# Kernel tuning notes

Measured on AMD Instinct MI355X. Metric: run time of the kernel, lower is better.

The kernel has to match this reference:

```python
import jax, jax.numpy as jnp
import numpy as np

B, S, H, V, T = 512, 128, 1024, 4096, 32  # batch, enc len, hidden, output_size, max_length


def setup_inputs() -> dict:
    key = jax.random.key(0)
    ks = jax.random.split(key, 9)
    sc = 1.0 / np.sqrt(H).astype(np.float32)
    return {
        "encoder_outputs": jax.random.normal(ks[0], (B, S, H), jnp.float32),
        "sem_embs": jax.random.normal(ks[1], (B, S, H), jnp.float32),
        "embedding": jax.random.normal(ks[2], (V + 3, H), jnp.float32) * sc,
        "W_ih": jax.random.normal(ks[3], (3 * H, H), jnp.float32) * sc,
        "W_hh": jax.random.normal(ks[4], (3 * H, H), jnp.float32) * sc,
        "b_ih": jax.random.normal(ks[5], (3 * H,), jnp.float32) * sc,
        "b_hh": jax.random.normal(ks[6], (3 * H,), jnp.float32) * sc,
        "W_out": jax.random.normal(ks[7], (V, H), jnp.float32) * sc,
        "b_out": jax.random.normal(ks[8], (V,), jnp.float32) * sc,
    }


def gru_cell(x, h, W_ih, W_hh, b_ih, b_hh):
    # PyTorch GRU cell math: r,z,n gate order
    gi = x @ W_ih.T + b_ih
    gh = h @ W_hh.T + b_hh
    i_r, i_z, i_n = jnp.split(gi, 3, axis=-1)
    h_r, h_z, h_n = jnp.split(gh, 3, axis=-1)
    r = jax.nn.sigmoid(i_r + h_r)
    z = jax.nn.sigmoid(i_z + h_z)
    n = jnp.tanh(i_n + r * h_n)
    return (1.0 - z) * n + z * h


def reference(encoder_outputs, sem_embs, embedding, W_ih, W_hh, b_ih, b_hh, W_out, b_out):
    bs, _, hid = encoder_outputs.shape
    # init_batch: append fake EOS key/value embeddings (length mask is all-False -> no-op)
    fake_eos = jnp.broadcast_to(embedding[V][None, None, :], (bs, 1, hid))
    fake_eos_sem = jnp.broadcast_to(embedding[V + 1][None, None, :], (bs, 1, hid))
    keys = jnp.concatenate([encoder_outputs, fake_eos], axis=1)      # [B, S+1, H]
    values = jnp.concatenate([sem_embs, fake_eos_sem], axis=1)       # [B, S+1, H]
    scale = 1.0 / jnp.sqrt(jnp.asarray(hid, jnp.float32))

    def step(carry, _):
        tok, h = carry
        emb = embedding[tok]                                         # [B, H]
        h = gru_cell(emb, h, W_ih, W_hh, b_ih, b_hh)                 # [B, H]
        w = jax.nn.softmax(jnp.einsum('bh,bkh->bk', h, keys) * scale, axis=-1)  # [B, S+1]
        r = jnp.einsum('bk,bkh->bh', w, values)                      # [B, H]
        logits = (r + h) @ W_out.T + b_out                           # [B, V]
        logp = jax.nn.log_softmax(logits, axis=-1)
        x = jnp.argmax(logits, axis=-1)                              # eval-mode greedy decode
        lp = jnp.take_along_axis(logp, x[:, None], axis=-1)[:, 0]
        ent = -jnp.sum(jnp.exp(logp) * logp, axis=-1)
        return (x, h), (x, lp, ent, w)

    tok0 = jnp.full((bs,), V + 2, dtype=jnp.int32)  # SOS token = output_size + 2
    h0 = jnp.zeros((bs, hid), jnp.float32)
    _, (seq, lps, ents, ws) = jax.lax.scan(step, (tok0, h0), None, length=T)
    seq = jnp.moveaxis(seq, 0, 1)    # [B, T]
    lps = jnp.moveaxis(lps, 0, 1)
    ents = jnp.moveaxis(ents, 0, 1)
    ws = jnp.moveaxis(ws, 0, 1)      # [B, T, S+1]
    zf = jnp.zeros((bs, 1), jnp.float32)
    sequence = jnp.concatenate([seq, jnp.zeros((bs, 1), seq.dtype)], axis=-1)
    per_step_logits = jnp.concatenate([lps, zf], axis=-1)
    entropy = jnp.concatenate([ents, zf], axis=-1)
    return sequence, per_step_logits, entropy, ws
```

## Files before the change

### kernel.cpp

```cpp
#include <hip/hip_runtime.h>
#include <stdint.h>

#define HDIM 1024
#define NB   512
#define SEQ  128
#define VOUT 4096
#define TSTEPS 32
#define EROWS 4160

#define SEQ_OFF 0
#define LP_OFF  16896
#define ENT_OFF 33792
#define WS_OFF  50688

__global__ void init_kernel(float* __restrict__ h, int* __restrict__ tok,
                            float* __restrict__ out) {
  int idx = blockIdx.x * blockDim.x + threadIdx.x;
  h[idx] = 0.f;
  if (idx < NB) {
    tok[idx] = VOUT + 2;
    out[SEQ_OFF + idx * 33 + 32] = 0.f;
    out[LP_OFF  + idx * 33 + 32] = 0.f;
    out[ENT_OFF + idx * 33 + 32] = 0.f;
  }
}

__global__ __launch_bounds__(256) void gemm64_kernel(
    const float* __restrict__ A, const float* __restrict__ W,
    const float* __restrict__ bias, float* __restrict__ C,
    int N, int Mlim, int KLEN, int zstride) {
  __shared__ __align__(16) float Als[32][68];
  __shared__ __align__(16) float Bls[32][68];
  const int tid = threadIdx.x;
  const int tx = tid & 15, ty = tid >> 4;
  const int m0 = blockIdx.y * 64, n0 = blockIdx.x * 64;
  const int z = blockIdx.z;
  const int kbeg = z * KLEN;
  const int sr = tid >> 3;
  const int scol = (tid & 7) << 2;

  const int ca0 = sr ^ scol;
  const int ca1 = (sr + 32) ^ scol;

  const int ra = min(m0 + sr, Mlim - 1);
  const int rb = min(m0 + sr + 32, Mlim - 1);
  const float* a0 = A + (size_t)ra * HDIM + kbeg + scol;
  const float* a1 = A + (size_t)rb * HDIM + kbeg + scol;
  const float* w0 = W + (size_t)(n0 + sr) * HDIM + kbeg + scol;
  const float* w1 = W + (size_t)(n0 + sr + 32) * HDIM + kbeg + scol;

  float accT[4][4];
#pragma unroll
  for (int i = 0; i < 4; ++i)
#pragma unroll
    for (int j = 0; j < 4; ++j) accT[i][j] = 0.f;

  float4 av0 = *(const float4*)(a0);
  float4 av1 = *(const float4*)(a1);
  float4 wv0 = *(const float4*)(w0);
  float4 wv1 = *(const float4*)(w1);

  for (int k0 = 0; k0 < KLEN; k0 += 32) {
    __syncthreads();
    Als[scol + 0][ca0] = av0.x; Als[scol + 1][ca0] = av0.y;
    Als[scol + 2][ca0] = av0.z; Als[scol + 3][ca0] = av0.w;
    Als[scol + 0][ca1] = av1.x; Als[scol + 1][ca1] = av1.y;
    Als[scol + 2][ca1] = av1.z; Als[scol + 3][ca1] = av1.w;
    Bls[scol + 0][ca0] = wv0.x; Bls[scol + 1][ca0] = wv0.y;
    Bls[scol + 2][ca0] = wv0.z; Bls[scol + 3][ca0] = wv0.w;
    Bls[scol + 0][ca1] = wv1.x; Bls[scol + 1][ca1] = wv1.y;
    Bls[scol + 2][ca1] = wv1.z; Bls[scol + 3][ca1] = wv1.w;
    __syncthreads();

    {
      const int kn = min(k0 + 32, KLEN - 32);
      av0 = *(const float4*)(a0 + kn);
      av1 = *(const float4*)(a1 + kn);
      wv0 = *(const float4*)(w0 + kn);
      wv1 = *(const float4*)(w1 + kn);
    }

    float ac[4][4];
#pragma unroll
    for (int i = 0; i < 4; ++i)
#pragma unroll
      for (int j = 0; j < 4; ++j) ac[i][j] = 0.f;

#pragma unroll
    for (int kk = 0; kk < 32; ++kk) {
      const int sz = kk & 28;
      float4 a4 = *(const float4*)&Als[kk][(ty * 4) ^ sz];
      float4 b4 = *(const float4*)&Bls[kk][(tx * 4) ^ sz];
      float a_[4] = {a4.x, a4.y, a4.z, a4.w};
      float b_[4] = {b4.x, b4.y, b4.z, b4.w};
#pragma unroll
      for (int i = 0; i < 4; ++i)
#pragma unroll
        for (int j = 0; j < 4; ++j) ac[i][j] = fmaf(a_[i], b_[j], ac[i][j]);
    }
#pragma unroll
    for (int i = 0; i < 4; ++i)
#pragma unroll
      for (int j = 0; j < 4; ++j) accT[i][j] += ac[i][j];
  }

  float* Cz = C + (size_t)z * zstride;
  float b0 = 0.f, b1 = 0.f, b2 = 0.f, b3 = 0.f;
  if (z == 0) {
    b0 = bias[n0 + tx * 4 + 0];
    b1 = bias[n0 + tx * 4 + 1];
    b2 = bias[n0 + tx * 4 + 2];
    b3 = bias[n0 + tx * 4 + 3];
  }
#pragma unroll
  for (int i = 0; i < 4; ++i) {
    int m = m0 + ty * 4 + i;
    float4 o;
    o.x = accT[i][0] + b0;
    o.y = accT[i][1] + b1;
    o.z = accT[i][2] + b2;
    o.w = accT[i][3] + b3;
    *(float4*)&Cz[(size_t)m * N + n0 + tx * 4] = o;
  }
}

__global__ __launch_bounds__(256) void gate_kernel(
    const float* __restrict__ E2, const float* __restrict__ gh,
    const int* __restrict__ tok, float* __restrict__ h) {
  int idx = blockIdx.x * blockDim.x + threadIdx.x;
  int b = idx >> 8;
  int c = (idx & 255) << 2;
  const float* e = E2 + (size_t)tok[b] * (3 * HDIM) + c;
  const float* g0 = gh + (size_t)b * (3 * HDIM) + c;
  const float* g1 = g0 + (size_t)NB * 3 * HDIM;
  float4 ir = *(const float4*)(e);
  float4 iz = *(const float4*)(e + HDIM);
  float4 in_ = *(const float4*)(e + 2 * HDIM);
  float4 hra = *(const float4*)(g0);
  float4 hza = *(const float4*)(g0 + HDIM);
  float4 hna = *(const float4*)(g0 + 2 * HDIM);
  float4 hrb = *(const float4*)(g1);
  float4 hzb = *(const float4*)(g1 + HDIM);
  float4 hnb = *(const float4*)(g1 + 2 * HDIM);
  float4 hv = *(const float4*)&h[(size_t)b * HDIM + c];
  float4 o;
  {
    float r = 1.f / (1.f + expf(-(ir.x + hra.x + hrb.x)));
    float z = 1.f / (1.f + expf(-(iz.x + hza.x + hzb.x)));
    float n = tanhf(in_.x + r * (hna.x + hnb.x));
    o.x = (1.f - z) * n + z * hv.x;
  }
  {
    float r = 1.f / (1.f + expf(-(ir.y + hra.y + hrb.y)));
    float z = 1.f / (1.f + expf(-(iz.y + hza.y + hzb.y)));
    float n = tanhf(in_.y + r * (hna.y + hnb.y));
    o.y = (1.f - z) * n + z * hv.y;
  }
  {
    float r = 1.f / (1.f + expf(-(ir.z + hra.z + hrb.z)));
    float z = 1.f / (1.f + expf(-(iz.z + hza.z + hzb.z)));
    float n = tanhf(in_.z + r * (hna.z + hnb.z));
    o.z = (1.f - z) * n + z * hv.z;
  }
  {
    float r = 1.f / (1.f + expf(-(ir.w + hra.w + hrb.w)));
    float z = 1.f / (1.f + expf(-(iz.w + hza.w + hzb.w)));
    float n = tanhf(in_.w + r * (hna.w + hnb.w));
    o.w = (1.f - z) * n + z * hv.w;
  }
  *(float4*)&h[(size_t)b * HDIM + c] = o;
}

#define SMEM_BYTES 37440
__global__ __launch_bounds__(512) void attn_gh_kernel(
    const float* __restrict__ h, const float* __restrict__ enc,
    const float* __restrict__ sem, const float* __restrict__ emb,
    float* __restrict__ x, float* __restrict__ out, int t,
    const float* __restrict__ W_hh, const float* __restrict__ b_hh,
    float* __restrict__ gh, int nattn) {
  __shared__ __align__(16) char smem[SMEM_BYTES];
  const int tid = threadIdx.x;
  if ((int)blockIdx.x < nattn) {
    float* hs = reinterpret_cast<float*>(smem);
    float (*accb)[HDIM] = reinterpret_cast<float (*)[HDIM]>(smem + 4096);
    float* uls = reinterpret_cast<float*>(smem + 36864);
    float* usums = reinterpret_cast<float*>(smem + 37392);
    const int b = blockIdx.x;
    const int lane = tid & 63, wv = tid >> 6;

    *(float2*)&hs[tid * 2] = *(const float2*)&h[(size_t)b * HDIM + tid * 2];
    __syncthreads();

    const int l4 = lane * 4;
    float4 hv0 = *(const float4*)&hs[l4];
    float4 hv1 = *(const float4*)&hs[l4 + 256];
    float4 hv2 = *(const float4*)&hs[l4 + 512];
    float4 hv3 = *(const float4*)&hs[l4 + 768];

    float4 acc0 = {0, 0, 0, 0}, acc1 = {0, 0, 0, 0};
    float4 acc2 = {0, 0, 0, 0}, acc3 = {0, 0, 0, 0};
    float usum = 0.f;

    for (int k = wv; k < SEQ + 1; k += 8) {
      const float* kr;
      const float* vr;
      if (k < SEQ) {
        kr = enc + ((size_t)b * SEQ + k) * HDIM;
        vr = sem + ((size_t)b * SEQ + k) * HDIM;
      } else {
        kr = emb + (size_t)VOUT * HDIM;
        vr = emb + (size_t)(VOUT + 1) * HDIM;
      }
      float4 e0 = *(const float4*)(kr + l4);
      float4 e1 = *(const float4*)(kr + l4 + 256);
      float4 e2 = *(const float4*)(kr + l4 + 512);
      float4 e3 = *(const float4*)(kr + l4 + 768);
      float4 v0 = *(const float4*)(vr + l4);
      float4 v1 = *(const float4*)(vr + l4 + 256);
      float4 v2 = *(const float4*)(vr + l4 + 512);
      float4 v3 = *(const float4*)(vr + l4 + 768);

      float p = 0.f;
      p = fmaf(e0.x, hv0.x, p); p = fmaf(e0.y, hv0.y, p);
      p = fmaf(e0.z, hv0.z, p); p = fmaf(e0.w, hv0.w, p);
      p = fmaf(e1.x, hv1.x, p); p = fmaf(e1.y, hv1.y, p);
      p = fmaf(e1.z, hv1.z, p); p = fmaf(e1.w, hv1.w, p);
      p = fmaf(e2.x, hv2.x, p); p = fmaf(e2.y, hv2.y, p);
      p = fmaf(e2.z, hv2.z, p); p = fmaf(e2.w, hv2.w, p);
      p = fmaf(e3.x, hv3.x, p); p = fmaf(e3.y, hv3.y, p);
      p = fmaf(e3.z, hv3.z, p); p = fmaf(e3.w, hv3.w, p);
#pragma unroll
      for (int off = 32; off; off >>= 1) p += __shfl_xor(p, off);

      float u = expf(p * 0.03125f);
      usum += u;
      if (lane == 0) uls[k] = u;

      acc0.x = fmaf(u, v0.x, acc0.x); acc0.y = fmaf(u, v0.y, acc0.y);
      acc0.z = fmaf(u, v0.z, acc0.z); acc0.w = fmaf(u, v0.w, acc0.w);
      acc1.x = fmaf(u, v1.x, acc1.x); acc1.y = fmaf(u, v1.y, acc1.y);
      acc1.z = fmaf(u, v1.z, acc1.z); acc1.w = fmaf(u, v1.w, acc1.w);
      acc2.x = fmaf(u, v2.x, acc2.x); acc2.y = fmaf(u, v2.y, acc2.y);
      acc2.z = fmaf(u, v2.z, acc2.z); acc2.w = fmaf(u, v2.w, acc2.w);
      acc3.x = fmaf(u, v3.x, acc3.x); acc3.y = fmaf(u, v3.y, acc3.y);
      acc3.z = fmaf(u, v3.z, acc3.z); acc3.w = fmaf(u, v3.w, acc3.w);
    }

    if (lane == 0) usums[wv] = usum;
    *(float4*)&accb[wv][l4] = acc0;
    *(float4*)&accb[wv][l4 + 256] = acc1;
    *(float4*)&accb[wv][l4 + 512] = acc2;
    *(float4*)&accb[wv][l4 + 768] = acc3;
    __syncthreads();

    float U = 0.f;
#pragma unroll
    for (int w = 0; w < 8; ++w) U += usums[w];
    float rinv = 1.f / U;

#pragma unroll
    for (int dd = 0; dd < 2; ++dd) {
      int d = tid + dd * 512;
      float sum = 0.f;
#pragma unroll
      for (int w = 0; w < 8; ++w) sum += accb[w][d];
      x[(size_t)b * HDIM + d] = sum * rinv + hs[d];
    }

    if (tid < SEQ + 1)
      out[WS_OFF + ((size_t)b * TSTEPS + t) * (SEQ + 1) + tid] = uls[tid] * rinv;
  } else {
    float (*Als)[132] = reinterpret_cast<float (*)[132]>(smem);
    float (*Bls)[68] = reinterpret_cast<float (*)[68]>(smem + 16896);
    int gb = blockIdx.x - nattn;
    const int z = gb / 192; gb -= z * 192;
    const int by = gb / 48, bx = gb - by * 48;
    const int m0 = by * 128, n0 = bx * 64;
    const int kbeg = z * 512;
    const int tx = tid & 15, ty = tid >> 4;
    const int sr = tid >> 3;
    const int scol = (tid & 7) << 2;
    const int ca = sr ^ scol;

    const float* a0 = h + (size_t)(m0 + sr) * HDIM + kbeg + scol;
    const float* a1 = h + (size_t)(m0 + sr + 64) * HDIM + kbeg + scol;
    const float* w0 = W_hh + (size_t)(n0 + sr) * HDIM + kbeg + scol;

    float accT[4][4];
#pragma unroll
    for (int i = 0; i < 4; ++i)
#pragma unroll
      for (int j = 0; j < 4; ++j) accT[i][j] = 0.f;

    float4 av0 = *(const float4*)(a0);
    float4 av1 = *(const float4*)(a1);
    float4 wv0 = *(const float4*)(w0);

    for (int k0 = 0; k0 < 512; k0 += 32) {
      __syncthreads();
      Als[scol + 0][ca] = av0.x; Als[scol + 1][ca] = av0.y;
      Als[scol + 2][ca] = av0.z; Als[scol + 3][ca] = av0.w;
      Als[scol + 0][ca + 64] = av1.x; Als[scol + 1][ca + 64] = av1.y;
      Als[scol + 2][ca + 64] = av1.z; Als[scol + 3][ca + 64] = av1.w;
      Bls[scol + 0][ca] = wv0.x; Bls[scol + 1][ca] = wv0.y;
      Bls[scol + 2][ca] = wv0.z; Bls[scol + 3][ca] = wv0.w;
      __syncthreads();

      {
        const int kn = min(k0 + 32, 512 - 32);
        av0 = *(const float4*)(a0 + kn);
        av1 = *(const float4*)(a1 + kn);
        wv0 = *(const float4*)(w0 + kn);
      }

      float ac[4][4];
#pragma unroll
      for (int i = 0; i < 4; ++i)
#pragma unroll
        for (int j = 0; j < 4; ++j) ac[i][j] = 0.f;

#pragma unroll
      for (int kk = 0; kk < 32; ++kk) {
        const int sz = kk & 28;
        float4 a4 = *(const float4*)&Als[kk][(ty * 4) ^ sz];
        float4 b4 = *(const float4*)&Bls[kk][(tx * 4) ^ sz];
        float a_[4] = {a4.x, a4.y, a4.z, a4.w};
        float b_[4] = {b4.x, b4.y, b4.z, b4.w};
#pragma unroll
        for (int i = 0; i < 4; ++i)
#pragma unroll
          for (int j = 0; j < 4; ++j) ac[i][j] = fmaf(a_[i], b_[j], ac[i][j]);
      }
#pragma unroll
      for (int i = 0; i < 4; ++i)
#pragma unroll
        for (int j = 0; j < 4; ++j) accT[i][j] += ac[i][j];
    }

    float* Cz = gh + (size_t)z * (NB * 3 * HDIM);
    float b0 = 0.f, b1 = 0.f, b2 = 0.f, b3 = 0.f;
    if (z == 0) {
      b0 = b_hh[n0 + tx * 4 + 0];
      b1 = b_hh[n0 + tx * 4 + 1];
      b2 = b_hh[n0 + tx * 4 + 2];
      b3 = b_hh[n0 + tx * 4 + 3];
    }
#pragma unroll
    for (int i = 0; i < 4; ++i) {
      int m = m0 + ty * 4 + i;
      float4 o;
      o.x = accT[i][0] + b0;
      o.y = accT[i][1] + b1;
      o.z = accT[i][2] + b2;
      o.w = accT[i][3] + b3;
      *(float4*)&Cz[(size_t)m * (3 * HDIM) + n0 + tx * 4] = o;
    }
  }
}

__global__ __launch_bounds__(256) void finalgate_kernel(
    const float* __restrict__ logits, float* __restrict__ out, int t,
    const float* __restrict__ E2, const float* __restrict__ gh,
    float* __restrict__ h) {
  const int b = blockIdx.x, tid = threadIdx.x;
  const int lane = tid & 63, wv = tid >> 6;
  const float* lrow = logits + (size_t)b * VOUT;
  float m = -3.4e38f; int mi = 0;
  float s = 0.f, ts = 0.f;
#pragma unroll
  for (int it = 0; it < 4; ++it) {
    int j = (tid << 2) + (it << 10);
    float4 v = *(const float4*)&lrow[j];
    float e;
    e = expf(v.x); s += e; ts = fmaf(e, v.x, ts); if (v.x > m) { m = v.x; mi = j; }
    e = expf(v.y); s += e; ts = fmaf(e, v.y, ts); if (v.y > m) { m = v.y; mi = j + 1; }
    e = expf(v.z); s += e; ts = fmaf(e, v.z, ts); if (v.z > m) { m = v.z; mi = j + 2; }
    e = expf(v.w); s += e; ts = fmaf(e, v.w, ts); if (v.w > m) { m = v.w; mi = j + 3; }
  }
#pragma unroll
  for (int off = 32; off; off >>= 1) {
    float om = __shfl_xor(m, off);
    int oi = __shfl_xor(mi, off);
    s += __shfl_xor(s, off);
    ts += __shfl_xor(ts, off);
    if (om > m || (om == m && oi < mi)) { m = om; mi = oi; }
  }
  __shared__ float smx[4], ssm[4], sts[4];
  __shared__ int smi[4];
  __shared__ int mib;
  if (lane == 0) { smx[wv] = m; smi[wv] = mi; ssm[wv] = s; sts[wv] = ts; }
  __syncthreads();
  if (tid == 0) {
#pragma unroll
    for (int w = 1; w < 4; ++w) {
      s += ssm[w]; ts += sts[w];
      if (smx[w] > m || (smx[w] == m && smi[w] < mi)) { m = smx[w]; mi = smi[w]; }
    }
    float lse = logf(s);
    float lp = m - lse;
    float ent = lse - ts / s;
    out[SEQ_OFF + (size_t)b * 33 + t] = (float)mi;
    out[LP_OFF  + (size_t)b * 33 + t] = lp;
    out[ENT_OFF + (size_t)b * 33 + t] = ent;
    mib = mi;
  }
  __syncthreads();

  const int c = tid << 2;
  const float* e = E2 + (size_t)mib * (3 * HDIM) + c;
  const float* g0 = gh + (size_t)b * (3 * HDIM) + c;
  const float* g1 = g0 + (size_t)NB * 3 * HDIM;
  float4 ir = *(const float4*)(e);
  float4 iz = *(const float4*)(e + HDIM);
  float4 in_ = *(const float4*)(e + 2 * HDIM);
  float4 hra = *(const float4*)(g0);
  float4 hza = *(const float4*)(g0 + HDIM);
  float4 hna = *(const float4*)(g0 + 2 * HDIM);
  float4 hrb = *(const float4*)(g1);
  float4 hzb = *(const float4*)(g1 + HDIM);
  float4 hnb = *(const float4*)(g1 + 2 * HDIM);
  float4 hv = *(const float4*)&h[(size_t)b * HDIM + c];
  float4 o;
  {
    float r = 1.f / (1.f + expf(-(ir.x + hra.x + hrb.x)));
    float z = 1.f / (1.f + expf(-(iz.x + hza.x + hzb.x)));
    float n = tanhf(in_.x + r * (hna.x + hnb.x));
    o.x = (1.f - z) * n + z * hv.x;
  }
  {
    float r = 1.f / (1.f + expf(-(ir.y + hra.y + hrb.y)));
    float z = 1.f / (1.f + expf(-(iz.y + hza.y + hzb.y)));
    float n = tanhf(in_.y + r * (hna.y + hnb.y));
    o.y = (1.f - z) * n + z * hv.y;
  }
  {
    float r = 1.f / (1.f + expf(-(ir.z + hra.z + hrb.z)));
    float z = 1.f / (1.f + expf(-(iz.z + hza.z + hzb.z)));
    float n = tanhf(in_.z + r * (hna.z + hnb.z));
    o.z = (1.f - z) * n + z * hv.z;
  }
  {
    float r = 1.f / (1.f + expf(-(ir.w + hra.w + hrb.w)));
    float z = 1.f / (1.f + expf(-(iz.w + hza.w + hzb.w)));
    float n = tanhf(in_.w + r * (hna.w + hnb.w));
    o.w = (1.f - z) * n + z * hv.w;
  }
  *(float4*)&h[(size_t)b * HDIM + c] = o;
}

extern "C" void kernel_launch(void* const* d_in, const int* in_sizes, int n_in,
                              void* d_out, int out_size, void* d_ws, size_t ws_size,
                              hipStream_t stream) {
  const float* enc   = (const float*)d_in[0];
  const float* sem   = (const float*)d_in[1];
  const float* emb   = (const float*)d_in[2];
  const float* W_ih  = (const float*)d_in[3];
  const float* W_hh  = (const float*)d_in[4];
  const float* b_ih  = (const float*)d_in[5];
  const float* b_hh  = (const float*)d_in[6];
  const float* W_out = (const float*)d_in[7];
  const float* b_out = (const float*)d_in[8];
  float* out = (float*)d_out;

  float* h      = (float*)d_ws;
  float* x      = h + (size_t)NB * HDIM;
  float* gh     = x + (size_t)NB * HDIM;
  float* logits = gh + (size_t)2 * NB * 3 * HDIM;
  float* E2     = logits + (size_t)NB * VOUT;
  int*   tok    = (int*)(E2 + (size_t)EROWS * 3 * HDIM);

  init_kernel<<<2048, 256, 0, stream>>>(h, tok, out);
  gemm64_kernel<<<dim3(48, 65, 1), 256, 0, stream>>>(emb, W_ih, b_ih, E2,
                                                     3 * HDIM, VOUT + 3, HDIM, 0);
  attn_gh_kernel<<<384, 512, 0, stream>>>(h, enc, sem, emb, x, out, 0,
                                          W_hh, b_hh, gh, 0);
  gate_kernel<<<512, 256, 0, stream>>>(E2, gh, tok, h);

  for (int t = 0; t < TSTEPS; ++t) {
    attn_gh_kernel<<<896, 512, 0, stream>>>(h, enc, sem, emb, x, out, t,
                                            W_hh, b_hh, gh, 512);
    gemm64_kernel<<<dim3(64, 8, 1), 256, 0, stream>>>(x, W_out, b_out, logits,
                                                      VOUT, NB, HDIM, 0);
    finalgate_kernel<<<512, 256, 0, stream>>>(logits, out, t, E2, gh, h);
  }
}
```

Before: 7.520 ms.

## Use 128x64 GEMM tiles and split-K output projection summed in finalgate

The GEMM kernel now computes a 128x64 output tile per block (8x4 per thread), giving more register reuse of each B fragment and halving the block count for the embedding precompute. The per-step logits GEMM is split into two K halves over blockIdx.z, writing two partial buffers that finalgate sums while loading. This keeps the grid at 512 blocks despite the larger tiles, at the cost of an extra logits buffer read and write per step and higher register pressure.

```diff
diff --git a/kernel.cpp b/kernel.cpp
--- a/kernel.cpp
+++ b/kernel.cpp
@@ -25,81 +25,89 @@
   }
 }
 
-__global__ __launch_bounds__(256) void gemm64_kernel(
+__global__ __launch_bounds__(256) void gemm128_kernel(
     const float* __restrict__ A, const float* __restrict__ W,
     const float* __restrict__ bias, float* __restrict__ C,
     int N, int Mlim, int KLEN, int zstride) {
-  __shared__ __align__(16) float Als[32][68];
+  __shared__ __align__(16) float Als[32][132];
   __shared__ __align__(16) float Bls[32][68];
   const int tid = threadIdx.x;
   const int tx = tid & 15, ty = tid >> 4;
-  const int m0 = blockIdx.y * 64, n0 = blockIdx.x * 64;
+  const int m0 = blockIdx.y * 128, n0 = blockIdx.x * 64;
   const int z = blockIdx.z;
   const int kbeg = z * KLEN;
   const int sr = tid >> 3;
   const int scol = (tid & 7) << 2;
 
-  const int ca0 = sr ^ scol;
-  const int ca1 = (sr + 32) ^ scol;
-
-  const int ra = min(m0 + sr, Mlim - 1);
-  const int rb = min(m0 + sr + 32, Mlim - 1);
-  const float* a0 = A + (size_t)ra * HDIM + kbeg + scol;
-  const float* a1 = A + (size_t)rb * HDIM + kbeg + scol;
+  const int ca = sr ^ scol;
+
+  const float* a0 = A + (size_t)min(m0 + sr,      Mlim - 1) * HDIM + kbeg + scol;
+  const float* a1 = A + (size_t)min(m0 + sr + 32, Mlim - 1) * HDIM + kbeg + scol;
+  const float* a2 = A + (size_t)min(m0 + sr + 64, Mlim - 1) * HDIM + kbeg + scol;
+  const float* a3 = A + (size_t)min(m0 + sr + 96, Mlim - 1) * HDIM + kbeg + scol;
   const float* w0 = W + (size_t)(n0 + sr) * HDIM + kbeg + scol;
   const float* w1 = W + (size_t)(n0 + sr + 32) * HDIM + kbeg + scol;
 
-  float accT[4][4];
-#pragma unroll
-  for (int i = 0; i < 4; ++i)
+  float accT[8][4];
+#pragma unroll
+  for (int i = 0; i < 8; ++i)
 #pragma unroll
     for (int j = 0; j < 4; ++j) accT[i][j] = 0.f;
 
   float4 av0 = *(const float4*)(a0);
   float4 av1 = *(const float4*)(a1);
+  float4 av2 = *(const float4*)(a2);
+  float4 av3 = *(const float4*)(a3);
   float4 wv0 = *(const float4*)(w0);
   float4 wv1 = *(const float4*)(w1);
 
   for (int k0 = 0; k0 < KLEN; k0 += 32) {
     __syncthreads();
-    Als[scol + 0][ca0] = av0.x; Als[scol + 1][ca0] = av0.y;
-    Als[scol + 2][ca0] = av0.z; Als[scol + 3][ca0] = av0.w;
-    Als[scol + 0][ca1] = av1.x; Als[scol + 1][ca1] = av1.y;
-    Als[scol + 2][ca1] = av1.z; Als[scol + 3][ca1] = av1.w;
-    Bls[scol + 0][ca0] = wv0.x; Bls[scol + 1][ca0] = wv0.y;
-    Bls[scol + 2][ca0] = wv0.z; Bls[scol + 3][ca0] = wv0.w;
-    Bls[scol + 0][ca1] = wv1.x; Bls[scol + 1][ca1] = wv1.y;
-    Bls[scol + 2][ca1] = wv1.z; Bls[scol + 3][ca1] = wv1.w;
+    Als[scol + 0][ca] = av0.x; Als[scol + 1][ca] = av0.y;
+    Als[scol + 2][ca] = av0.z; Als[scol + 3][ca] = av0.w;
+    Als[scol + 0][ca + 32] = av1.x; Als[scol + 1][ca + 32] = av1.y;
+    Als[scol + 2][ca + 32] = av1.z; Als[scol + 3][ca + 32] = av1.w;
+    Als[scol + 0][ca + 64] = av2.x; Als[scol + 1][ca + 64] = av2.y;
+    Als[scol + 2][ca + 64] = av2.z; Als[scol + 3][ca + 64] = av2.w;
+    Als[scol + 0][ca + 96] = av3.x; Als[scol + 1][ca + 96] = av3.y;
+    Als[scol + 2][ca + 96] = av3.z; Als[scol + 3][ca + 96] = av3.w;
+    Bls[scol + 0][ca] = wv0.x; Bls[scol + 1][ca] = wv0.y;
+    Bls[scol + 2][ca] = wv0.z; Bls[scol + 3][ca] = wv0.w;
+    Bls[scol + 0][ca + 32] = wv1.x; Bls[scol + 1][ca + 32] = wv1.y;
+    Bls[scol + 2][ca + 32] = wv1.z; Bls[scol + 3][ca + 32] = wv1.w;
     __syncthreads();
 
     {
       const int kn = min(k0 + 32, KLEN - 32);
       av0 = *(const float4*)(a0 + kn);
       av1 = *(const float4*)(a1 + kn);
+      av2 = *(const float4*)(a2 + kn);
+      av3 = *(const float4*)(a3 + kn);
       wv0 = *(const float4*)(w0 + kn);
       wv1 = *(const float4*)(w1 + kn);
     }
 
-    float ac[4][4];
-#pragma unroll
-    for (int i = 0; i < 4; ++i)
+    float ac[8][4];
+#pragma unroll
+    for (int i = 0; i < 8; ++i)
 #pragma unroll
       for (int j = 0; j < 4; ++j) ac[i][j] = 0.f;
 
 #pragma unroll
     for (int kk = 0; kk < 32; ++kk) {
       const int sz = kk & 28;
-      float4 a4 = *(const float4*)&Als[kk][(ty * 4) ^ sz];
-      float4 b4 = *(const float4*)&Bls[kk][(tx * 4) ^ sz];
-      float a_[4] = {a4.x, a4.y, a4.z, a4.w};
+      float4 aLo = *(const float4*)&Als[kk][(ty * 4) ^ sz];
+      float4 aHi = *(const float4*)&Als[kk][64 + ((ty * 4) ^ sz)];
+      float4 b4  = *(const float4*)&Bls[kk][(tx * 4) ^ sz];
+      float a_[8] = {aLo.x, aLo.y, aLo.z, aLo.w, aHi.x, aHi.y, aHi.z, aHi.w};
       float b_[4] = {b4.x, b4.y, b4.z, b4.w};
 #pragma unroll
-      for (int i = 0; i < 4; ++i)
+      for (int i = 0; i < 8; ++i)
 #pragma unroll
         for (int j = 0; j < 4; ++j) ac[i][j] = fmaf(a_[i], b_[j], ac[i][j]);
     }
 #pragma unroll
-    for (int i = 0; i < 4; ++i)
+    for (int i = 0; i < 8; ++i)
 #pragma unroll
       for (int j = 0; j < 4; ++j) accT[i][j] += ac[i][j];
   }
@@ -113,14 +121,18 @@
     b3 = bias[n0 + tx * 4 + 3];
   }
 #pragma unroll
-  for (int i = 0; i < 4; ++i) {
-    int m = m0 + ty * 4 + i;
-    float4 o;
-    o.x = accT[i][0] + b0;
-    o.y = accT[i][1] + b1;
-    o.z = accT[i][2] + b2;
-    o.w = accT[i][3] + b3;
-    *(float4*)&Cz[(size_t)m * N + n0 + tx * 4] = o;
+  for (int q = 0; q < 2; ++q) {
+#pragma unroll
+    for (int i = 0; i < 4; ++i) {
+      int m = m0 + q * 64 + ty * 4 + i;
+      if (m >= Mlim) continue;
+      float4 o;
+      o.x = accT[q * 4 + i][0] + b0;
+      o.y = accT[q * 4 + i][1] + b1;
+      o.z = accT[q * 4 + i][2] + b2;
+      o.w = accT[q * 4 + i][3] + b3;
+      *(float4*)&Cz[(size_t)m * N + n0 + tx * 4] = o;
+    }
   }
 }
 
@@ -364,13 +376,17 @@
     float* __restrict__ h) {
   const int b = blockIdx.x, tid = threadIdx.x;
   const int lane = tid & 63, wv = tid >> 6;
-  const float* lrow = logits + (size_t)b * VOUT;
+  const float* lrow0 = logits + (size_t)b * VOUT;
+  const float* lrow1 = lrow0 + (size_t)NB * VOUT;
   float m = -3.4e38f; int mi = 0;
   float s = 0.f, ts = 0.f;
 #pragma unroll
   for (int it = 0; it < 4; ++it) {
     int j = (tid << 2) + (it << 10);
-    float4 v = *(const float4*)&lrow[j];
+    float4 va = *(const float4*)&lrow0[j];
+    float4 vb = *(const float4*)&lrow1[j];
+    float4 v;
+    v.x = va.x + vb.x; v.y = va.y + vb.y; v.z = va.z + vb.z; v.w = va.w + vb.w;
     float e;
     e = expf(v.x); s += e; ts = fmaf(e, v.x, ts); if (v.x > m) { m = v.x; mi = j; }
     e = expf(v.y); s += e; ts = fmaf(e, v.y, ts); if (v.y > m) { m = v.y; mi = j + 1; }
@@ -466,12 +482,12 @@
   float* x      = h + (size_t)NB * HDIM;
   float* gh     = x + (size_t)NB * HDIM;
   float* logits = gh + (size_t)2 * NB * 3 * HDIM;
-  float* E2     = logits + (size_t)NB * VOUT;
+  float* E2     = logits + (size_t)2 * NB * VOUT;
   int*   tok    = (int*)(E2 + (size_t)EROWS * 3 * HDIM);
 
   init_kernel<<<2048, 256, 0, stream>>>(h, tok, out);
-  gemm64_kernel<<<dim3(48, 65, 1), 256, 0, stream>>>(emb, W_ih, b_ih, E2,
-                                                     3 * HDIM, VOUT + 3, HDIM, 0);
+  gemm128_kernel<<<dim3(48, 33, 1), 256, 0, stream>>>(emb, W_ih, b_ih, E2,
+                                                      3 * HDIM, VOUT + 3, HDIM, 0);
   attn_gh_kernel<<<384, 512, 0, stream>>>(h, enc, sem, emb, x, out, 0,
                                           W_hh, b_hh, gh, 0);
   gate_kernel<<<512, 256, 0, stream>>>(E2, gh, tok, h);
@@ -479,8 +495,9 @@
   for (int t = 0; t < TSTEPS; ++t) {
     attn_gh_kernel<<<896, 512, 0, stream>>>(h, enc, sem, emb, x, out, t,
                                             W_hh, b_hh, gh, 512);
-    gemm64_kernel<<<dim3(64, 8, 1), 256, 0, stream>>>(x, W_out, b_out, logits,
-                                                      VOUT, NB, HDIM, 0);
+    gemm128_kernel<<<dim3(64, 4, 2), 256, 0, stream>>>(x, W_out, b_out, logits,
+                                                       VOUT, NB, HDIM / 2,
+                                                       NB * VOUT);
     finalgate_kernel<<<512, 256, 0, stream>>>(logits, out, t, E2, gh, h);
   }
 }
```

After: 7.098 ms. -5.6%, faster.

## Double-buffer GEMM shared tiles and split-K the output projection

Applied to the files above, without the earlier changes.

The 64x64 GEMM now double-buffers its shared-memory tiles, leaving one barrier per K step instead of two. The per-step output-projection GEMM is split into two K halves across blockIdx.z, writing two partial logit buffers. The final softmax/argmax kernel sums them on load. This doubles the block count of the small 512-block projection GEMM to fill more CUs, at the cost of extra logits traffic and workspace.

```diff
diff --git a/kernel.cpp b/kernel.cpp
--- a/kernel.cpp
+++ b/kernel.cpp
@@ -29,8 +29,8 @@
     const float* __restrict__ A, const float* __restrict__ W,
     const float* __restrict__ bias, float* __restrict__ C,
     int N, int Mlim, int KLEN, int zstride) {
-  __shared__ __align__(16) float Als[32][68];
-  __shared__ __align__(16) float Bls[32][68];
+  __shared__ __align__(16) float Als[2][32][68];
+  __shared__ __align__(16) float Bls[2][32][68];
   const int tid = threadIdx.x;
   const int tx = tid & 15, ty = tid >> 4;
   const int m0 = blockIdx.y * 64, n0 = blockIdx.x * 64;
@@ -59,21 +59,38 @@
   float4 av1 = *(const float4*)(a1);
   float4 wv0 = *(const float4*)(w0);
   float4 wv1 = *(const float4*)(w1);
-
+  Als[0][scol + 0][ca0] = av0.x; Als[0][scol + 1][ca0] = av0.y;
+  Als[0][scol + 2][ca0] = av0.z; Als[0][scol + 3][ca0] = av0.w;
+  Als[0][scol + 0][ca1] = av1.x; Als[0][scol + 1][ca1] = av1.y;
+  Als[0][scol + 2][ca1] = av1.z; Als[0][scol + 3][ca1] = av1.w;
+  Bls[0][scol + 0][ca0] = wv0.x; Bls[0][scol + 1][ca0] = wv0.y;
+  Bls[0][scol + 2][ca0] = wv0.z; Bls[0][scol + 3][ca0] = wv0.w;
+  Bls[0][scol + 0][ca1] = wv1.x; Bls[0][scol + 1][ca1] = wv1.y;
+  Bls[0][scol + 2][ca1] = wv1.z; Bls[0][scol + 3][ca1] = wv1.w;
+  {
+    const int kn = min(32, KLEN - 32);
+    av0 = *(const float4*)(a0 + kn);
+    av1 = *(const float4*)(a1 + kn);
+    wv0 = *(const float4*)(w0 + kn);
+    wv1 = *(const float4*)(w1 + kn);
+  }
+  __syncthreads();
+
+  int cur = 0;
   for (int k0 = 0; k0 < KLEN; k0 += 32) {
-    __syncthreads();
-    Als[scol + 0][ca0] = av0.x; Als[scol + 1][ca0] = av0.y;
-    Als[scol + 2][ca0] = av0.z; Als[scol + 3][ca0] = av0.w;
-    Als[scol + 0][ca1] = av1.x; Als[scol + 1][ca1] = av1.y;
-    Als[scol + 2][ca1] = av1.z; Als[scol + 3][ca1] = av1.w;
-    Bls[scol + 0][ca0] = wv0.x; Bls[scol + 1][ca0] = wv0.y;
-    Bls[scol + 2][ca0] = wv0.z; Bls[scol + 3][ca0] = wv0.w;
-    Bls[scol + 0][ca1] = wv1.x; Bls[scol + 1][ca1] = wv1.y;
-    Bls[scol + 2][ca1] = wv1.z; Bls[scol + 3][ca1] = wv1.w;
-    __syncthreads();
-
+    if (k0 + 32 < KLEN) {
+      const int nx = cur ^ 1;
+      Als[nx][scol + 0][ca0] = av0.x; Als[nx][scol + 1][ca0] = av0.y;
+      Als[nx][scol + 2][ca0] = av0.z; Als[nx][scol + 3][ca0] = av0.w;
+      Als[nx][scol + 0][ca1] = av1.x; Als[nx][scol + 1][ca1] = av1.y;
+      Als[nx][scol + 2][ca1] = av1.z; Als[nx][scol + 3][ca1] = av1.w;
+      Bls[nx][scol + 0][ca0] = wv0.x; Bls[nx][scol + 1][ca0] = wv0.y;
+      Bls[nx][scol + 2][ca0] = wv0.z; Bls[nx][scol + 3][ca0] = wv0.w;
+      Bls[nx][scol + 0][ca1] = wv1.x; Bls[nx][scol + 1][ca1] = wv1.y;
+      Bls[nx][scol + 2][ca1] = wv1.z; Bls[nx][scol + 3][ca1] = wv1.w;
+    }
     {
-      const int kn = min(k0 + 32, KLEN - 32);
+      const int kn = min(k0 + 64, KLEN - 32);
       av0 = *(const float4*)(a0 + kn);
       av1 = *(const float4*)(a1 + kn);
       wv0 = *(const float4*)(w0 + kn);
@@ -89,8 +106,8 @@
 #pragma unroll
     for (int kk = 0; kk < 32; ++kk) {
       const int sz = kk & 28;
-      float4 a4 = *(const float4*)&Als[kk][(ty * 4) ^ sz];
-      float4 b4 = *(const float4*)&Bls[kk][(tx * 4) ^ sz];
+      float4 a4 = *(const float4*)&Als[cur][kk][(ty * 4) ^ sz];
+      float4 b4 = *(const float4*)&Bls[cur][kk][(tx * 4) ^ sz];
       float a_[4] = {a4.x, a4.y, a4.z, a4.w};
       float b_[4] = {b4.x, b4.y, b4.z, b4.w};
 #pragma unroll
@@ -102,6 +119,9 @@
     for (int i = 0; i < 4; ++i)
 #pragma unroll
       for (int j = 0; j < 4; ++j) accT[i][j] += ac[i][j];
+
+    __syncthreads();
+    cur ^= 1;
   }
 
   float* Cz = C + (size_t)z * zstride;
@@ -364,13 +384,17 @@
     float* __restrict__ h) {
   const int b = blockIdx.x, tid = threadIdx.x;
   const int lane = tid & 63, wv = tid >> 6;
-  const float* lrow = logits + (size_t)b * VOUT;
+  const float* lrow0 = logits + (size_t)b * VOUT;
+  const float* lrow1 = lrow0 + (size_t)NB * VOUT;
   float m = -3.4e38f; int mi = 0;
   float s = 0.f, ts = 0.f;
 #pragma unroll
   for (int it = 0; it < 4; ++it) {
     int j = (tid << 2) + (it << 10);
-    float4 v = *(const float4*)&lrow[j];
+    float4 va = *(const float4*)&lrow0[j];
+    float4 vb = *(const float4*)&lrow1[j];
+    float4 v;
+    v.x = va.x + vb.x; v.y = va.y + vb.y; v.z = va.z + vb.z; v.w = va.w + vb.w;
     float e;
     e = expf(v.x); s += e; ts = fmaf(e, v.x, ts); if (v.x > m) { m = v.x; mi = j; }
     e = expf(v.y); s += e; ts = fmaf(e, v.y, ts); if (v.y > m) { m = v.y; mi = j + 1; }
@@ -466,7 +490,7 @@
   float* x      = h + (size_t)NB * HDIM;
   float* gh     = x + (size_t)NB * HDIM;
   float* logits = gh + (size_t)2 * NB * 3 * HDIM;
-  float* E2     = logits + (size_t)NB * VOUT;
+  float* E2     = logits + (size_t)2 * NB * VOUT;
   int*   tok    = (int*)(E2 + (size_t)EROWS * 3 * HDIM);
 
   init_kernel<<<2048, 256, 0, stream>>>(h, tok, out);
@@ -479,8 +503,9 @@
   for (int t = 0; t < TSTEPS; ++t) {
     attn_gh_kernel<<<896, 512, 0, stream>>>(h, enc, sem, emb, x, out, t,
                                             W_hh, b_hh, gh, 512);
-    gemm64_kernel<<<dim3(64, 8, 1), 256, 0, stream>>>(x, W_out, b_out, logits,
-                                                      VOUT, NB, HDIM, 0);
+    gemm64_kernel<<<dim3(64, 8, 2), 256, 0, stream>>>(x, W_out, b_out, logits,
+                                                      VOUT, NB, HDIM / 2,
+                                                      NB * VOUT);
     finalgate_kernel<<<512, 256, 0, stream>>>(logits, out, t, E2, gh, h);
   }
 }
```

Result: faster. 7.189 ms (-4.4%).

## Split-K output GEMM into two partial buffers and software-pipeline attention loads

Applied to the files above, without the earlier changes.

The output projection GEMM now runs with a z-dimension of 2. Each z-slice handles half of the K dimension and writes its own partial logits buffer, and finalgate sums the two partials on load. This doubles the block count of a small 512-block GEMM to fill more CUs, at the cost of extra logits traffic. Separately, the attention loop now gives each wave a contiguous run of 16 encoder rows and prefetches the next row's key/value float4s while computing the current one, with the fake-EOS row handled by wave 0 afterwards. This is meant to hide global load latency.

```diff
diff --git a/kernel.cpp b/kernel.cpp
--- a/kernel.cpp
+++ b/kernel.cpp
@@ -201,24 +201,29 @@
     float4 acc2 = {0, 0, 0, 0}, acc3 = {0, 0, 0, 0};
     float usum = 0.f;
 
-    for (int k = wv; k < SEQ + 1; k += 8) {
-      const float* kr;
-      const float* vr;
-      if (k < SEQ) {
-        kr = enc + ((size_t)b * SEQ + k) * HDIM;
-        vr = sem + ((size_t)b * SEQ + k) * HDIM;
-      } else {
-        kr = emb + (size_t)VOUT * HDIM;
-        vr = emb + (size_t)(VOUT + 1) * HDIM;
-      }
-      float4 e0 = *(const float4*)(kr + l4);
-      float4 e1 = *(const float4*)(kr + l4 + 256);
-      float4 e2 = *(const float4*)(kr + l4 + 512);
-      float4 e3 = *(const float4*)(kr + l4 + 768);
-      float4 v0 = *(const float4*)(vr + l4);
-      float4 v1 = *(const float4*)(vr + l4 + 256);
-      float4 v2 = *(const float4*)(vr + l4 + 512);
-      float4 v3 = *(const float4*)(vr + l4 + 768);
+    const float* erow = enc + ((size_t)b * SEQ + wv * 16) * HDIM + l4;
+    const float* vrow = sem + ((size_t)b * SEQ + wv * 16) * HDIM + l4;
+
+    float4 e0 = *(const float4*)(erow);
+    float4 e1 = *(const float4*)(erow + 256);
+    float4 e2 = *(const float4*)(erow + 512);
+    float4 e3 = *(const float4*)(erow + 768);
+    float4 v0 = *(const float4*)(vrow);
+    float4 v1 = *(const float4*)(vrow + 256);
+    float4 v2 = *(const float4*)(vrow + 512);
+    float4 v3 = *(const float4*)(vrow + 768);
+
+#pragma unroll 2
+    for (int j = 0; j < 16; ++j) {
+      const size_t noff = (size_t)(j < 15 ? j + 1 : 15) * HDIM;
+      float4 f0 = *(const float4*)(erow + noff);
+      float4 f1 = *(const float4*)(erow + noff + 256);
+      float4 f2 = *(const float4*)(erow + noff + 512);
+      float4 f3 = *(const float4*)(erow + noff + 768);
+      float4 g0 = *(const float4*)(vrow + noff);
+      float4 g1 = *(const float4*)(vrow + noff + 256);
+      float4 g2 = *(const float4*)(vrow + noff + 512);
+      float4 g3 = *(const float4*)(vrow + noff + 768);
 
       float p = 0.f;
       p = fmaf(e0.x, hv0.x, p); p = fmaf(e0.y, hv0.y, p);
@@ -234,7 +239,7 @@
 
       float u = expf(p * 0.03125f);
       usum += u;
-      if (lane == 0) uls[k] = u;
+      if (lane == 0) uls[wv * 16 + j] = u;
 
       acc0.x = fmaf(u, v0.x, acc0.x); acc0.y = fmaf(u, v0.y, acc0.y);
       acc0.z = fmaf(u, v0.z, acc0.z); acc0.w = fmaf(u, v0.w, acc0.w);
@@ -244,6 +249,44 @@
       acc2.z = fmaf(u, v2.z, acc2.z); acc2.w = fmaf(u, v2.w, acc2.w);
       acc3.x = fmaf(u, v3.x, acc3.x); acc3.y = fmaf(u, v3.y, acc3.y);
       acc3.z = fmaf(u, v3.z, acc3.z); acc3.w = fmaf(u, v3.w, acc3.w);
+
+      e0 = f0; e1 = f1; e2 = f2; e3 = f3;
+      v0 = g0; v1 = g1; v2 = g2; v3 = g3;
+    }
+
+    if (wv == 0) {
+      const float* kr = emb + (size_t)VOUT * HDIM + l4;
+      const float* vr = emb + (size_t)(VOUT + 1) * HDIM + l4;
+      float4 q0 = *(const float4*)(kr);
+      float4 q1 = *(const float4*)(kr + 256);
+      float4 q2 = *(const float4*)(kr + 512);
+      float4 q3 = *(const float4*)(kr + 768);
+      float4 w0_ = *(const float4*)(vr);
+      float4 w1_ = *(const float4*)(vr + 256);
+      float4 w2_ = *(const float4*)(vr + 512);
+      float4 w3_ = *(const float4*)(vr + 768);
+      float p = 0.f;
+      p = fmaf(q0.x, hv0.x, p); p = fmaf(q0.y, hv0.y, p);
+      p = fmaf(q0.z, hv0.z, p); p = fmaf(q0.w, hv0.w, p);
+      p = fmaf(q1.x, hv1.x, p); p = fmaf(q1.y, hv1.y, p);
+      p = fmaf(q1.z, hv1.z, p); p = fmaf(q1.w, hv1.w, p);
+      p = fmaf(q2.x, hv2.x, p); p = fmaf(q2.y, hv2.y, p);
+      p = fmaf(q2.z, hv2.z, p); p = fmaf(q2.w, hv2.w, p);
+      p = fmaf(q3.x, hv3.x, p); p = fmaf(q3.y, hv3.y, p);
+      p = fmaf(q3.z, hv3.z, p); p = fmaf(q3.w, hv3.w, p);
+#pragma unroll
+      for (int off = 32; off; off >>= 1) p += __shfl_xor(p, off);
+      float u = expf(p * 0.03125f);
+      usum += u;
+      if (lane == 0) uls[SEQ] = u;
+      acc0.x = fmaf(u, w0_.x, acc0.x); acc0.y = fmaf(u, w0_.y, acc0.y);
+      acc0.z = fmaf(u, w0_.z, acc0.z); acc0.w = fmaf(u, w0_.w, acc0.w);
+      acc1.x = fmaf(u, w1_.x, acc1.x); acc1.y = fmaf(u, w1_.y, acc1.y);
+      acc1.z = fmaf(u, w1_.z, acc1.z); acc1.w = fmaf(u, w1_.w, acc1.w);
+      acc2.x = fmaf(u, w2_.x, acc2.x); acc2.y = fmaf(u, w2_.y, acc2.y);
+      acc2.z = fmaf(u, w2_.z, acc2.z); acc2.w = fmaf(u, w2_.w, acc2.w);
+      acc3.x = fmaf(u, w3_.x, acc3.x); acc3.y = fmaf(u, w3_.y, acc3.y);
+      acc3.z = fmaf(u, w3_.z, acc3.z); acc3.w = fmaf(u, w3_.w, acc3.w);
     }
 
     if (lane == 0) usums[wv] = usum;
@@ -364,13 +407,17 @@
     float* __restrict__ h) {
   const int b = blockIdx.x, tid = threadIdx.x;
   const int lane = tid & 63, wv = tid >> 6;
-  const float* lrow = logits + (size_t)b * VOUT;
+  const float* lrow0 = logits + (size_t)b * VOUT;
+  const float* lrow1 = lrow0 + (size_t)NB * VOUT;
   float m = -3.4e38f; int mi = 0;
   float s = 0.f, ts = 0.f;
 #pragma unroll
   for (int it = 0; it < 4; ++it) {
     int j = (tid << 2) + (it << 10);
-    float4 v = *(const float4*)&lrow[j];
+    float4 va = *(const float4*)&lrow0[j];
+    float4 vb = *(const float4*)&lrow1[j];
+    float4 v;
+    v.x = va.x + vb.x; v.y = va.y + vb.y; v.z = va.z + vb.z; v.w = va.w + vb.w;
     float e;
     e = expf(v.x); s += e; ts = fmaf(e, v.x, ts); if (v.x > m) { m = v.x; mi = j; }
     e = expf(v.y); s += e; ts = fmaf(e, v.y, ts); if (v.y > m) { m = v.y; mi = j + 1; }
@@ -466,7 +513,7 @@
   float* x      = h + (size_t)NB * HDIM;
   float* gh     = x + (size_t)NB * HDIM;
   float* logits = gh + (size_t)2 * NB * 3 * HDIM;
-  float* E2     = logits + (size_t)NB * VOUT;
+  float* E2     = logits + (size_t)2 * NB * VOUT;
   int*   tok    = (int*)(E2 + (size_t)EROWS * 3 * HDIM);
 
   init_kernel<<<2048, 256, 0, stream>>>(h, tok, out);
@@ -479,8 +526,9 @@
   for (int t = 0; t < TSTEPS; ++t) {
     attn_gh_kernel<<<896, 512, 0, stream>>>(h, enc, sem, emb, x, out, t,
                                             W_hh, b_hh, gh, 512);
-    gemm64_kernel<<<dim3(64, 8, 1), 256, 0, stream>>>(x, W_out, b_out, logits,
-                                                      VOUT, NB, HDIM, 0);
+    gemm64_kernel<<<dim3(64, 8, 2), 256, 0, stream>>>(x, W_out, b_out, logits,
+                                                      VOUT, NB, HDIM / 2,
+                                                      NB * VOUT);
     finalgate_kernel<<<512, 256, 0, stream>>>(logits, out, t, E2, gh, h);
   }
 }
```

Result: slower. 8.000 ms (+6.4%).
